# Performance work log

Hardware: AMD Instinct MI355X
Metric: run time of the kernel (lower is better)

The kernel has to match this reference:

```python
import jax, jax.numpy as jnp
import numpy as np

N = 50000      # num nodes
E = 800000     # num edges (avg degree 16)
F = 128        # node_features
H = 128        # hidden_channels
EPS = 1e-5     # BatchNorm eps


def setup_inputs() -> dict:
    key = jax.random.key(0)
    ks = jax.random.split(key, 16)
    s = 0.05
    return {
        "x": jax.random.normal(ks[0], (N, F), jnp.float32),
        "edge_index": jax.random.randint(ks[1], (2, E), 0, N, dtype=jnp.int32),
        # GCNConv 1
        "W1": jax.random.normal(ks[2], (F, H), jnp.float32) * s,
        "b1": jnp.zeros((H,), jnp.float32),
        "g1": jnp.ones((H,), jnp.float32),
        "be1": jnp.zeros((H,), jnp.float32),
        "m1": jax.random.normal(ks[3], (H,), jnp.float32) * 0.1,
        "v1": jnp.ones((H,), jnp.float32),
        # GCNConv 2
        "W2": jax.random.normal(ks[4], (H, H), jnp.float32) * s,
        "b2": jnp.zeros((H,), jnp.float32),
        "g2": jnp.ones((H,), jnp.float32),
        "be2": jnp.zeros((H,), jnp.float32),
        "m2": jax.random.normal(ks[5], (H,), jnp.float32) * 0.1,
        "v2": jnp.ones((H,), jnp.float32),
        # edge predictor MLP: Linear(2H->H) -> ReLU -> Linear(H->1)
        "epW1": jax.random.normal(ks[6], (2 * H, H), jnp.float32) * s,
        "epb1": jnp.zeros((H,), jnp.float32),
        "epW2": jax.random.normal(ks[7], (H, 1), jnp.float32) * s,
        "epb2": jnp.zeros((1,), jnp.float32),
    }


def gcn_layer(x, W, b, src, dst, n):
    """PyG GCNConv: add self-loops, symmetric D^-1/2 (A+I) D^-1/2 normalization."""
    xw = x @ W                               # [N, H]
    loop = jnp.arange(n, dtype=src.dtype)
    s = jnp.concatenate([src, loop])         # [E+N]
    d = jnp.concatenate([dst, loop])
    deg = jax.ops.segment_sum(jnp.ones_like(d, x.dtype), d, num_segments=n)
    dinv = jax.lax.rsqrt(deg)                # deg >= 1 (self-loops)
    norm = dinv[s] * dinv[d]                 # [E+N]
    out = jax.ops.segment_sum(norm[:, None] * xw[s], d, num_segments=n)  # [N, H]
    return out + b


def bn_eval(x, g, be, m, v):
    return (x - m) * (g * jax.lax.rsqrt(v + EPS)) + be


def reference(x, edge_index, W1, b1, g1, be1, m1, v1, W2, b2, g2, be2, m2, v2,
              epW1, epb1, epW2, epb2):
    src, dst = edge_index[0], edge_index[1]
    # two stacked GCNConv + BatchNorm (eval) + ReLU (dropout off in eval)
    h = jax.nn.relu(bn_eval(gcn_layer(x, W1, b1, src, dst, N), g1, be1, m1, v1))
    h = jax.nn.relu(bn_eval(gcn_layer(h, W2, b2, src, dst, N), g2, be2, m2, v2))
    # predict_link on the same edges: gather + concat + MLP + sigmoid
    h_edge = jnp.concatenate([h[src], h[dst]], axis=1)   # [E, 2H]
    z = jax.nn.relu(h_edge @ epW1 + epb1) @ epW2 + epb2  # [E, 1]
    return jax.nn.sigmoid(z).squeeze(-1)                 # [E]
```

## Files before the change

kernel.cpp:

```cpp
#include <hip/hip_runtime.h>
#include <math.h>

#define BN_EPS 1e-5f

typedef unsigned short u16;
typedef unsigned int u32;
typedef unsigned char u8;
typedef __attribute__((ext_vector_type(8))) short bf16x8;
typedef __attribute__((ext_vector_type(4))) float f32x4;
typedef __attribute__((ext_vector_type(2))) float f32x2;

__device__ __forceinline__ u16 f2bf(float f) {
  u32 u = __float_as_uint(f);
  u32 r = (u + 0x7fffu + ((u >> 16) & 1u)) >> 16;
  return (u16)r;
}
__device__ __forceinline__ u32 packbf2(float x, float y) {
  return (u32)f2bf(x) | ((u32)f2bf(y) << 16);
}
__device__ __forceinline__ float lo_bf(u32 p) { return __uint_as_float(p << 16); }
__device__ __forceinline__ float hi_bf(u32 p) { return __uint_as_float(p & 0xffff0000u); }

__device__ __forceinline__ void unpack8(uint4 p, float* f) {
  f[0] = lo_bf(p.x); f[1] = hi_bf(p.x);
  f[2] = lo_bf(p.y); f[3] = hi_bf(p.y);
  f[4] = lo_bf(p.z); f[5] = hi_bf(p.z);
  f[6] = lo_bf(p.w); f[7] = hi_bf(p.w);
}

__device__ __forceinline__ void unpack_fp8x4(u32 p, float* f) {
  f32x2 lo = __builtin_amdgcn_cvt_pk_f32_fp8((int)p, false);
  f32x2 hi = __builtin_amdgcn_cvt_pk_f32_fp8((int)p, true);
  f[0] = lo.x; f[1] = lo.y; f[2] = hi.x; f[3] = hi.y;
}
__device__ __forceinline__ u8 f2fp8(float o) {
  u32 pk = __builtin_amdgcn_cvt_pk_fp8_f32(o, o, 0, false);
  return (u8)(pk & 0xffu);
}

__global__ __launch_bounds__(256) void clear_k(int* __restrict__ p, int n) {
  int i = blockIdx.x * 256 + threadIdx.x;
  if (i < n) p[i] = 0;
}

__global__ __launch_bounds__(256) void count_pos_k(const int* __restrict__ dst,
                                                   int* __restrict__ cnt,
                                                   int* __restrict__ pintra,
                                                   int T, int E) {
  int t = blockIdx.x * 256 + threadIdx.x;
  if (t >= T) return;
  int e0 = t, e1 = t + T, e2 = t + 2 * T, e3 = t + 3 * T;
  int d0 = (e0 < E) ? dst[e0] : -1;
  int d1 = (e1 < E) ? dst[e1] : -1;
  int d2 = (e2 < E) ? dst[e2] : -1;
  int d3 = (e3 < E) ? dst[e3] : -1;
  int p0 = (d0 >= 0) ? atomicAdd(&cnt[d0], 1) : 0;
  int p1 = (d1 >= 0) ? atomicAdd(&cnt[d1], 1) : 0;
  int p2 = (d2 >= 0) ? atomicAdd(&cnt[d2], 1) : 0;
  int p3 = (d3 >= 0) ? atomicAdd(&cnt[d3], 1) : 0;
  if (d0 >= 0) pintra[e0] = p0;
  if (d1 >= 0) pintra[e1] = p1;
  if (d2 >= 0) pintra[e2] = p2;
  if (d3 >= 0) pintra[e3] = p3;
}

__global__ __launch_bounds__(256) void blocksum_k(const int* __restrict__ cnt,
                                                  int* __restrict__ bsum, int n) {
  __shared__ int red[256];
  int tid = threadIdx.x;
  int i = blockIdx.x * 256 + tid;
  int v = (i < n) ? cnt[i] : 0;
  red[tid] = v;
  __syncthreads();
  for (int o = 128; o > 0; o >>= 1) {
    if (tid < o) red[tid] += red[tid + o];
    __syncthreads();
  }
  if (tid == 0) bsum[blockIdx.x] = red[0];
}

__global__ __launch_bounds__(1024) void scan_bsum_k(int* __restrict__ bsum, int nb) {
  __shared__ int part[1024];
  int tid = threadIdx.x;
  int v = (tid < nb) ? bsum[tid] : 0;
  part[tid] = v;
  __syncthreads();
  for (int o = 1; o < 1024; o <<= 1) {
    int t = (tid >= o) ? part[tid - o] : 0;
    __syncthreads();
    part[tid] += t;
    __syncthreads();
  }
  if (tid < nb) bsum[tid] = part[tid] - v;
}

__global__ __launch_bounds__(256) void scan_final_k(const int* __restrict__ cnt,
                                                    const int* __restrict__ bsum,
                                                    int* __restrict__ rowptr,
                                                    float* __restrict__ dinv, int n) {
  __shared__ int part[256];
  int tid = threadIdx.x;
  int i = blockIdx.x * 256 + tid;
  int v = (i < n) ? cnt[i] : 0;
  part[tid] = v;
  __syncthreads();
  for (int o = 1; o < 256; o <<= 1) {
    int t = (tid >= o) ? part[tid - o] : 0;
    __syncthreads();
    part[tid] += t;
    __syncthreads();
  }
  if (i < n) {
    int excl = part[tid] - v + bsum[blockIdx.x];
    rowptr[i] = excl;
    dinv[i] = rsqrtf((float)(v + 1));
    if (i == n - 1) rowptr[n] = excl + v;
  }
}

__global__ __launch_bounds__(256) void fill_csr_k(const int* __restrict__ src,
                                                  const int* __restrict__ dst,
                                                  const int* __restrict__ rowptr,
                                                  const int* __restrict__ pintra,
                                                  int* __restrict__ csrS, int T, int E) {
  int t = blockIdx.x * 256 + threadIdx.x;
  if (t >= T) return;
  #pragma unroll
  for (int u = 0; u < 4; ++u) {
    int e = t + u * T;
    if (e < E) {
      int d = dst[e];
      int p = rowptr[d] + pintra[e];
      csrS[p] = src[e];
    }
  }
}

__global__ __launch_bounds__(256) void prep_k(const float* __restrict__ W1,
    const float* __restrict__ W2, const float* __restrict__ epW1,
    const float* __restrict__ b1, const float* __restrict__ g1,
    const float* __restrict__ be1, const float* __restrict__ m1,
    const float* __restrict__ v1,
    const float* __restrict__ b2, const float* __restrict__ g2,
    const float* __restrict__ be2, const float* __restrict__ m2,
    const float* __restrict__ v2,
    u16* __restrict__ wout, float* __restrict__ bnout) {
  if (blockIdx.x < 256) {
    int t = blockIdx.x * 256 + threadIdx.x;
    int m = t >> 14, r = t & 16383;
    int n = r >> 7, k = r & 127;
    const float* src = (m == 0) ? W1 : (m == 1) ? W2 : epW1 + (size_t)(m - 2) * 16384;
    wout[t] = f2bf(src[k * 128 + n]);
  } else {
    int t = threadIdx.x;
    int layer = t >> 7, c = t & 127;
    const float* bb = layer ? b2 : b1;
    const float* gg = layer ? g2 : g1;
    const float* ee = layer ? be2 : be1;
    const float* mm = layer ? m2 : m1;
    const float* vv = layer ? v2 : v1;
    float alpha = gg[c] * rsqrtf(vv[c] + BN_EPS);
    float beta = (bb[c] - mm[c]) * alpha + ee[c];
    bnout[layer * 256 + c] = alpha;
    bnout[layer * 256 + 128 + c] = beta;
  }
}

template<bool BF16IN, bool SCALE, bool FP8OUT>
__global__ __launch_bounds__(256) void gemm_mfma_k(const void* __restrict__ Xv,
    const u16* __restrict__ Wt, const float* __restrict__ dinv,
    void* __restrict__ Yv, int M) {
  __shared__ u16 Xs[64][136];
  __shared__ u16 Ws[128][136];
  int tid = threadIdx.x;
  int row0 = blockIdx.x * 64;
  for (int i = tid; i < 2048; i += 256) {
    int n = i >> 4, c8 = i & 15;
    uint4 v = ((const uint4*)Wt)[i];
    *(uint4*)&Ws[n][c8 * 8] = v;
  }
  for (int i = tid; i < 1024; i += 256) {
    int r = i >> 4, c8 = i & 15;
    int gr = row0 + r;
    uint4 v = make_uint4(0u, 0u, 0u, 0u);
    if (gr < M) {
      if (BF16IN) {
        v = ((const uint4*)Xv)[(size_t)gr * 16 + c8];
      } else {
        const float* Xf = (const float*)Xv;
        float4 f0 = ((const float4*)Xf)[(size_t)gr * 32 + c8 * 2];
        float4 f1 = ((const float4*)Xf)[(size_t)gr * 32 + c8 * 2 + 1];
        v.x = packbf2(f0.x, f0.y); v.y = packbf2(f0.z, f0.w);
        v.z = packbf2(f1.x, f1.y); v.w = packbf2(f1.z, f1.w);
      }
    }
    *(uint4*)&Xs[r][c8 * 8] = v;
  }
  __syncthreads();
  int w = tid >> 6, l = tid & 63;
  int lr = l & 15, kq = l >> 4;
  bf16x8 a[4];
  #pragma unroll
  for (int kk = 0; kk < 4; ++kk)
    a[kk] = *(const bf16x8*)&Xs[w * 16 + lr][kk * 32 + kq * 8];
  float sc[4];
  #pragma unroll
  for (int r = 0; r < 4; ++r) {
    int grow = row0 + w * 16 + kq * 4 + r;
    sc[r] = (SCALE && grow < M) ? dinv[grow] : 1.f;
  }
  #pragma unroll
  for (int ct = 0; ct < 8; ++ct) {
    f32x4 c = {0.f, 0.f, 0.f, 0.f};
    #pragma unroll
    for (int kk = 0; kk < 4; ++kk) {
      bf16x8 b = *(const bf16x8*)&Ws[ct * 16 + lr][kk * 32 + kq * 8];
      c = __builtin_amdgcn_mfma_f32_16x16x32_bf16(a[kk], b, c, 0, 0, 0);
    }
    int n = ct * 16 + lr;
    #pragma unroll
    for (int r = 0; r < 4; ++r) {
      int grow = row0 + w * 16 + kq * 4 + r;
      if (grow < M) {
        float o = c[r];
        if (SCALE) o *= sc[r];
        if (FP8OUT) {
          ((u8*)Yv)[(size_t)grow * 128 + n] = f2fp8(o);
        } else {
          ((u16*)Yv)[(size_t)grow * 128 + n] = f2bf(o);
        }
      }
    }
  }
}

__global__ __launch_bounds__(256) void gemm_mfma2_k(const u16* __restrict__ X,
    const u16* __restrict__ WtA, const u16* __restrict__ WtB,
    const float* __restrict__ bias, u8* __restrict__ YA8, u16* __restrict__ YB, int M) {
  __shared__ u16 Xs[64][136];
  __shared__ u16 Ws[128][136];
  int tid = threadIdx.x;
  int row0 = blockIdx.x * 64;
  for (int i = tid; i < 1024; i += 256) {
    int r = i >> 4, c8 = i & 15;
    int gr = row0 + r;
    uint4 v = make_uint4(0u, 0u, 0u, 0u);
    if (gr < M) v = ((const uint4*)X)[(size_t)gr * 16 + c8];
    *(uint4*)&Xs[r][c8 * 8] = v;
  }
  __syncthreads();
  int w = tid >> 6, l = tid & 63;
  int lr = l & 15, kq = l >> 4;
  bf16x8 a[4];
  #pragma unroll
  for (int kk = 0; kk < 4; ++kk)
    a[kk] = *(const bf16x8*)&Xs[w * 16 + lr][kk * 32 + kq * 8];

  for (int m = 0; m < 2; ++m) {
    const u16* Wt = m ? WtB : WtA;
    __syncthreads();
    for (int i = tid; i < 2048; i += 256) {
      int n = i >> 4, c8 = i & 15;
      uint4 v = ((const uint4*)Wt)[i];
      *(uint4*)&Ws[n][c8 * 8] = v;
    }
    __syncthreads();
    #pragma unroll
    for (int ct = 0; ct < 8; ++ct) {
      f32x4 c = {0.f, 0.f, 0.f, 0.f};
      #pragma unroll
      for (int kk = 0; kk < 4; ++kk) {
        bf16x8 b = *(const bf16x8*)&Ws[ct * 16 + lr][kk * 32 + kq * 8];
        c = __builtin_amdgcn_mfma_f32_16x16x32_bf16(a[kk], b, c, 0, 0, 0);
      }
      int n = ct * 16 + lr;
      if (m == 0) {
        float bv = bias[n];
        #pragma unroll
        for (int r = 0; r < 4; ++r) {
          int grow = row0 + w * 16 + kq * 4 + r;
          if (grow < M) YA8[(size_t)grow * 128 + n] = f2fp8(c[r] + bv);
        }
      } else {
        #pragma unroll
        for (int r = 0; r < 4; ++r) {
          int grow = row0 + w * 16 + kq * 4 + r;
          if (grow < M) YB[(size_t)grow * 128 + n] = f2bf(c[r]);
        }
      }
    }
  }
}

__global__ __launch_bounds__(256) void agg_bn_relu_k(const u8* __restrict__ XW8,
    const int* __restrict__ rowptr, const int* __restrict__ csrS,
    const float* __restrict__ dinv, const float* __restrict__ ab,
    uint4* __restrict__ H4, int n) {
  int node = (blockIdx.x * 256 + threadIdx.x) >> 4;
  if (node >= n) return;
  int l16 = threadIdx.x & 15;
  int beg = rowptr[node], end = rowptr[node + 1];
  const uint2* X2 = (const uint2*)XW8;
  float ac[8];
  #pragma unroll
  for (int j = 0; j < 8; ++j) ac[j] = 0.f;
  float f[8];
  for (int i = beg; i < end; i += 8) {
    int s[8];
    bool h[8];
    #pragma unroll
    for (int u = 0; u < 8; ++u) {
      int idx = i + u;
      h[u] = idx < end;
      s[u] = h[u] ? csrS[idx] : csrS[i];
    }
    uint2 p[8];
    #pragma unroll
    for (int u = 0; u < 8; ++u) p[u] = X2[(size_t)s[u] * 16 + l16];
    #pragma unroll
    for (int u = 0; u < 8; ++u) {
      if (h[u]) {
        unpack_fp8x4(p[u].x, f); unpack_fp8x4(p[u].y, f + 4);
        #pragma unroll
        for (int j = 0; j < 8; ++j) ac[j] += f[j];
      }
    }
  }
  {
    uint2 p = X2[(size_t)node * 16 + l16];
    unpack_fp8x4(p.x, f); unpack_fp8x4(p.y, f + 4);
    #pragma unroll
    for (int j = 0; j < 8; ++j) ac[j] += f[j];
  }
  float dn = dinv[node];
  int c = l16 * 8;
  float4 a0 = *(const float4*)&ab[c];
  float4 a1 = *(const float4*)&ab[c + 4];
  float4 t0 = *(const float4*)&ab[128 + c];
  float4 t1 = *(const float4*)&ab[128 + c + 4];
  float al[8] = {a0.x, a0.y, a0.z, a0.w, a1.x, a1.y, a1.z, a1.w};
  float bt[8] = {t0.x, t0.y, t0.z, t0.w, t1.x, t1.y, t1.z, t1.w};
  u32 out[4];
  #pragma unroll
  for (int j2 = 0; j2 < 4; ++j2) {
    float o0 = fmaxf(fmaf(ac[2*j2]     * dn, al[2*j2],     bt[2*j2]),     0.f);
    float o1 = fmaxf(fmaf(ac[2*j2 + 1] * dn, al[2*j2 + 1], bt[2*j2 + 1]), 0.f);
    out[j2] = packbf2(o0, o1);
  }
  H4[(size_t)node * 16 + l16] = make_uint4(out[0], out[1], out[2], out[3]);
}

__global__ __launch_bounds__(256) void edge_pass_k(const u8* __restrict__ A8,
    const uint4* __restrict__ B4, const int* __restrict__ rowptr,
    const int* __restrict__ csrS, const float* __restrict__ w2,
    float* __restrict__ pout, int n) {
  int node = (blockIdx.x * 256 + threadIdx.x) >> 6;
  if (node >= n) return;
  int lane = threadIdx.x & 63;
  int sub = lane >> 4, l16 = lane & 15;
  int beg = rowptr[node], end = rowptr[node + 1];
  if (beg >= end) return;
  float bvals[8];
  unpack8(B4[(size_t)node * 16 + l16], bvals);
  int c = l16 * 8;
  float4 w0 = *(const float4*)&w2[c];
  float4 w1 = *(const float4*)&w2[c + 4];
  float wv[8] = {w0.x, w0.y, w0.z, w0.w, w1.x, w1.y, w1.z, w1.w};
  const uint2* A2 = (const uint2*)A8;
  for (int i = beg + sub; i < end; i += 16) {
    int i1 = i + 4, i2 = i + 8, i3 = i + 12;
    bool h1 = i1 < end, h2 = i2 < end, h3 = i3 < end;
    int s0 = csrS[i];
    int s1 = h1 ? csrS[i1] : s0;
    int s2 = h2 ? csrS[i2] : s0;
    int s3 = h3 ? csrS[i3] : s0;
    uint2 pa0 = A2[(size_t)s0 * 16 + l16];
    uint2 pa1 = A2[(size_t)s1 * 16 + l16];
    uint2 pa2 = A2[(size_t)s2 * 16 + l16];
    uint2 pa3 = A2[(size_t)s3 * 16 + l16];
    float f[8];
    float dot0 = 0.f, dot1 = 0.f, dot2 = 0.f, dot3 = 0.f;
    unpack_fp8x4(pa0.x, f); unpack_fp8x4(pa0.y, f + 4);
    #pragma unroll
    for (int j = 0; j < 8; ++j) dot0 = fmaf(fmaxf(f[j] + bvals[j], 0.f), wv[j], dot0);
    unpack_fp8x4(pa1.x, f); unpack_fp8x4(pa1.y, f + 4);
    #pragma unroll
    for (int j = 0; j < 8; ++j) dot1 = fmaf(fmaxf(f[j] + bvals[j], 0.f), wv[j], dot1);
    unpack_fp8x4(pa2.x, f); unpack_fp8x4(pa2.y, f + 4);
    #pragma unroll
    for (int j = 0; j < 8; ++j) dot2 = fmaf(fmaxf(f[j] + bvals[j], 0.f), wv[j], dot2);
    unpack_fp8x4(pa3.x, f); unpack_fp8x4(pa3.y, f + 4);
    #pragma unroll
    for (int j = 0; j < 8; ++j) dot3 = fmaf(fmaxf(f[j] + bvals[j], 0.f), wv[j], dot3);
    #pragma unroll
    for (int o = 1; o <= 8; o <<= 1) {
      dot0 += __shfl_xor(dot0, o);
      dot1 += __shfl_xor(dot1, o);
      dot2 += __shfl_xor(dot2, o);
      dot3 += __shfl_xor(dot3, o);
    }
    if (l16 == 0) {
      pout[i] = dot0;
      if (h1) pout[i1] = dot1;
      if (h2) pout[i2] = dot2;
      if (h3) pout[i3] = dot3;
    }
  }
}

__global__ __launch_bounds__(256) void edge_fin_k(const float* __restrict__ pout,
    const int* __restrict__ dst, const int* __restrict__ pintra,
    const int* __restrict__ rowptr, const float* __restrict__ b2,
    float* __restrict__ out, int E) {
  int t = blockIdx.x * 256 + threadIdx.x;
  if (t >= E) return;
  int p = rowptr[dst[t]] + pintra[t];
  float z = pout[p] + b2[0];
  out[t] = 1.f / (1.f + expf(-z));
}

extern "C" void kernel_launch(void* const* d_in, const int* in_sizes, int n_in,
                              void* d_out, int out_size, void* d_ws, size_t ws_size,
                              hipStream_t stream) {
  const float* x    = (const float*)d_in[0];
  const int*   ei   = (const int*)d_in[1];
  const float* W1   = (const float*)d_in[2];
  const float* b1   = (const float*)d_in[3];
  const float* g1   = (const float*)d_in[4];
  const float* be1  = (const float*)d_in[5];
  const float* m1   = (const float*)d_in[6];
  const float* v1   = (const float*)d_in[7];
  const float* W2   = (const float*)d_in[8];
  const float* b2   = (const float*)d_in[9];
  const float* g2   = (const float*)d_in[10];
  const float* be2  = (const float*)d_in[11];
  const float* m2   = (const float*)d_in[12];
  const float* v2   = (const float*)d_in[13];
  const float* epW1 = (const float*)d_in[14];
  const float* epb1 = (const float*)d_in[15];
  const float* epW2 = (const float*)d_in[16];
  const float* epb2 = (const float*)d_in[17];

  int N = in_sizes[0] / 128;
  int E = in_sizes[1] / 2;
  const int* src = ei;
  const int* dst = ei + E;

  char* w = (char*)d_ws;
  size_t off = 0;
  auto carve = [&](size_t bytes) {
    void* p = w + off;
    off = (off + bytes + 255) & ~(size_t)255;
    return p;
  };
  u8*  bufX8 = (u8*)carve((size_t)N * 128);
  u16* bufH  = (u16*)carve((size_t)N * 128 * 2);
  u16* bufB  = (u16*)carve((size_t)N * 128 * 2);
  u8*  bufA8 = (u8*)carve((size_t)N * 128);
  int*   cnt   = (int*)carve((size_t)N * 4);
  int*   pintra= (int*)carve((size_t)E * 4);
  int*   rowptr= (int*)carve((size_t)(N + 1) * 4);
  float* dinv  = (float*)carve((size_t)N * 4);
  int*   csrS  = (int*)carve((size_t)E * 4);
  int*   bsum  = (int*)carve((size_t)1024 * 4);
  u16*   wsT   = (u16*)carve((size_t)4 * 16384 * 2);
  float* pout  = (float*)carve((size_t)E * 4);
  float* bnab  = (float*)carve((size_t)512 * 4);
  (void)ws_size; (void)n_in; (void)out_size;

  int nb = (N + 255) / 256;
  int T = (E + 3) / 4;
  int tb = (T + 255) / 256;

  clear_k<<<nb, 256, 0, stream>>>(cnt, N);
  prep_k<<<257, 256, 0, stream>>>(W1, W2, epW1, b1, g1, be1, m1, v1,
                                  b2, g2, be2, m2, v2, wsT, bnab);
  count_pos_k<<<tb, 256, 0, stream>>>(dst, cnt, pintra, T, E);
  blocksum_k<<<nb, 256, 0, stream>>>(cnt, bsum, N);
  scan_bsum_k<<<1, 1024, 0, stream>>>(bsum, nb);
  scan_final_k<<<nb, 256, 0, stream>>>(cnt, bsum, rowptr, dinv, N);
  fill_csr_k<<<tb, 256, 0, stream>>>(src, dst, rowptr, pintra, csrS, T, E);

  int gb = (N + 63) / 64;
  int an = (N + 15) / 16;
  int ab = (N + 3) / 4;
  const u16* WtW1 = wsT;
  const u16* WtW2 = wsT + 16384;
  const u16* WtA  = wsT + 2 * 16384;
  const u16* WtB  = wsT + 3 * 16384;

  gemm_mfma_k<false, true, true><<<gb, 256, 0, stream>>>(x, WtW1, dinv, bufX8, N);
  agg_bn_relu_k<<<an, 256, 0, stream>>>(bufX8, rowptr, csrS, dinv, bnab,
                                        (uint4*)bufH, N);
  gemm_mfma_k<true, true, true><<<gb, 256, 0, stream>>>(bufH, WtW2, dinv, bufX8, N);
  agg_bn_relu_k<<<an, 256, 0, stream>>>(bufX8, rowptr, csrS, dinv, bnab + 256,
                                        (uint4*)bufH, N);
  gemm_mfma2_k<<<gb, 256, 0, stream>>>(bufH, WtA, WtB, epb1, bufA8, bufB, N);
  edge_pass_k<<<ab, 256, 0, stream>>>(bufA8, (const uint4*)bufB, rowptr, csrS,
                                      epW2, pout, N);
  edge_fin_k<<<(E + 255) / 256, 256, 0, stream>>>(pout, dst, pintra, rowptr,
                                                  epb2, (float*)d_out, E);
}
```

Before: 211.1 us.

## Replicate degree counters eightfold to reduce atomic contention in CSR build

Edge counting now spreads atomics over eight replicated counter arrays chosen by edge index, then a new row-sum kernel turns them into per-replica prefix offsets plus total degree and dinv. CSR fill and the final edge output add the replica offset when computing positions. The aim is to cut same-address atomic serialization in count_pos. The cost is an extra kernel launch, 8x larger counter clearing, and an extra gather in fill_csr and edge_fin.

```diff
diff --git a/kernel.cpp b/kernel.cpp
--- a/kernel.cpp
+++ b/kernel.cpp
@@ -44,24 +44,34 @@
 }
 
 __global__ __launch_bounds__(256) void count_pos_k(const int* __restrict__ dst,
-                                                   int* __restrict__ cnt,
+                                                   int* __restrict__ cntR,
                                                    int* __restrict__ pintra,
-                                                   int T, int E) {
-  int t = blockIdx.x * 256 + threadIdx.x;
-  if (t >= T) return;
-  int e0 = t, e1 = t + T, e2 = t + 2 * T, e3 = t + 3 * T;
-  int d0 = (e0 < E) ? dst[e0] : -1;
-  int d1 = (e1 < E) ? dst[e1] : -1;
-  int d2 = (e2 < E) ? dst[e2] : -1;
-  int d3 = (e3 < E) ? dst[e3] : -1;
-  int p0 = (d0 >= 0) ? atomicAdd(&cnt[d0], 1) : 0;
-  int p1 = (d1 >= 0) ? atomicAdd(&cnt[d1], 1) : 0;
-  int p2 = (d2 >= 0) ? atomicAdd(&cnt[d2], 1) : 0;
-  int p3 = (d3 >= 0) ? atomicAdd(&cnt[d3], 1) : 0;
-  if (d0 >= 0) pintra[e0] = p0;
-  if (d1 >= 0) pintra[e1] = p1;
-  if (d2 >= 0) pintra[e2] = p2;
-  if (d3 >= 0) pintra[e3] = p3;
+                                                   int N, int E) {
+  int e = blockIdx.x * 256 + threadIdx.x;
+  if (e >= E) return;
+  int d = dst[e];
+  int r = e & 7;
+  int p = atomicAdd(&cntR[(size_t)r * N + d], 1);
+  pintra[e] = p;
+}
+
+__global__ __launch_bounds__(256) void rowsum_k(int* __restrict__ cntR,
+                                                int* __restrict__ cnt,
+                                                float* __restrict__ dinv, int N) {
+  int i = blockIdx.x * 256 + threadIdx.x;
+  if (i >= N) return;
+  int c[8];
+  #pragma unroll
+  for (int r = 0; r < 8; ++r) c[r] = cntR[(size_t)r * N + i];
+  int run = 0;
+  #pragma unroll
+  for (int r = 0; r < 8; ++r) {
+    int v = c[r];
+    cntR[(size_t)r * N + i] = run;
+    run += v;
+  }
+  cnt[i] = run;
+  dinv[i] = rsqrtf((float)(run + 1));
 }
 
 __global__ __launch_bounds__(256) void blocksum_k(const int* __restrict__ cnt,
@@ -96,8 +106,7 @@
 
 __global__ __launch_bounds__(256) void scan_final_k(const int* __restrict__ cnt,
                                                     const int* __restrict__ bsum,
-                                                    int* __restrict__ rowptr,
-                                                    float* __restrict__ dinv, int n) {
+                                                    int* __restrict__ rowptr, int n) {
   __shared__ int part[256];
   int tid = threadIdx.x;
   int i = blockIdx.x * 256 + tid;
@@ -113,7 +122,6 @@
   if (i < n) {
     int excl = part[tid] - v + bsum[blockIdx.x];
     rowptr[i] = excl;
-    dinv[i] = rsqrtf((float)(v + 1));
     if (i == n - 1) rowptr[n] = excl + v;
   }
 }
@@ -121,8 +129,10 @@
 __global__ __launch_bounds__(256) void fill_csr_k(const int* __restrict__ src,
                                                   const int* __restrict__ dst,
                                                   const int* __restrict__ rowptr,
+                                                  const int* __restrict__ cntR,
                                                   const int* __restrict__ pintra,
-                                                  int* __restrict__ csrS, int T, int E) {
+                                                  int* __restrict__ csrS,
+                                                  int N, int T, int E) {
   int t = blockIdx.x * 256 + threadIdx.x;
   if (t >= T) return;
   #pragma unroll
@@ -130,7 +140,8 @@
     int e = t + u * T;
     if (e < E) {
       int d = dst[e];
-      int p = rowptr[d] + pintra[e];
+      int r = e & 7;
+      int p = rowptr[d] + cntR[(size_t)r * N + d] + pintra[e];
       csrS[p] = src[e];
     }
   }
@@ -410,11 +421,13 @@
 
 __global__ __launch_bounds__(256) void edge_fin_k(const float* __restrict__ pout,
     const int* __restrict__ dst, const int* __restrict__ pintra,
-    const int* __restrict__ rowptr, const float* __restrict__ b2,
-    float* __restrict__ out, int E) {
+    const int* __restrict__ rowptr, const int* __restrict__ cntR,
+    const float* __restrict__ b2, float* __restrict__ out, int N, int E) {
   int t = blockIdx.x * 256 + threadIdx.x;
   if (t >= E) return;
-  int p = rowptr[dst[t]] + pintra[t];
+  int d = dst[t];
+  int r = t & 7;
+  int p = rowptr[d] + cntR[(size_t)r * N + d] + pintra[t];
   float z = pout[p] + b2[0];
   out[t] = 1.f / (1.f + expf(-z));
 }
@@ -457,6 +470,7 @@
   u16* bufH  = (u16*)carve((size_t)N * 128 * 2);
   u16* bufB  = (u16*)carve((size_t)N * 128 * 2);
   u8*  bufA8 = (u8*)carve((size_t)N * 128);
+  int*   cntR  = (int*)carve((size_t)8 * N * 4);
   int*   cnt   = (int*)carve((size_t)N * 4);
   int*   pintra= (int*)carve((size_t)E * 4);
   int*   rowptr= (int*)carve((size_t)(N + 1) * 4);
@@ -471,15 +485,18 @@
   int nb = (N + 255) / 256;
   int T = (E + 3) / 4;
   int tb = (T + 255) / 256;
-
-  clear_k<<<nb, 256, 0, stream>>>(cnt, N);
+  int eb = (E + 255) / 256;
+  int rb = (8 * N + 255) / 256;
+
+  clear_k<<<rb, 256, 0, stream>>>(cntR, 8 * N);
   prep_k<<<257, 256, 0, stream>>>(W1, W2, epW1, b1, g1, be1, m1, v1,
                                   b2, g2, be2, m2, v2, wsT, bnab);
-  count_pos_k<<<tb, 256, 0, stream>>>(dst, cnt, pintra, T, E);
+  count_pos_k<<<eb, 256, 0, stream>>>(dst, cntR, pintra, N, E);
+  rowsum_k<<<nb, 256, 0, stream>>>(cntR, cnt, dinv, N);
   blocksum_k<<<nb, 256, 0, stream>>>(cnt, bsum, N);
   scan_bsum_k<<<1, 1024, 0, stream>>>(bsum, nb);
-  scan_final_k<<<nb, 256, 0, stream>>>(cnt, bsum, rowptr, dinv, N);
-  fill_csr_k<<<tb, 256, 0, stream>>>(src, dst, rowptr, pintra, csrS, T, E);
+  scan_final_k<<<nb, 256, 0, stream>>>(cnt, bsum, rowptr, N);
+  fill_csr_k<<<tb, 256, 0, stream>>>(src, dst, rowptr, cntR, pintra, csrS, N, T, E);
 
   int gb = (N + 63) / 64;
   int an = (N + 15) / 16;
@@ -498,6 +515,6 @@
   gemm_mfma2_k<<<gb, 256, 0, stream>>>(bufH, WtA, WtB, epb1, bufA8, bufB, N);
   edge_pass_k<<<ab, 256, 0, stream>>>(bufA8, (const uint4*)bufB, rowptr, csrS,
                                       epW2, pout, N);
-  edge_fin_k<<<(E + 255) / 256, 256, 0, stream>>>(pout, dst, pintra, rowptr,
-                                                  epb2, (float*)d_out, E);
-}
+  edge_fin_k<<<eb, 256, 0, stream>>>(pout, dst, pintra, rowptr, cntR,
+                                     epb2, (float*)d_out, N, E);
+}
```

Result: slower. 221.7 us (+5.0%).
